# Optimization experiments

Measured on AMD Instinct MI355X. Metric: run time of the kernel, lower is better.

Reference implementation:

```python
import jax, jax.numpy as jnp
import numpy as np
import math

B, S, D = 4, 1024, 512
H, DK, DV = 8, 64, 64
NEG = -1.0e9
LN_EPS = 1e-5


def setup_inputs() -> dict:
    key = jax.random.key(0)
    ks = jax.random.split(key, 12)
    sc = 1.0 / math.sqrt(D)
    inp = {
        "input_Q": jax.random.normal(ks[0], (B, S, D), jnp.float32),
        "input_K": jax.random.normal(ks[1], (B, S, D), jnp.float32),
        "input_V": jax.random.normal(ks[2], (B, S, D), jnp.float32),
        "attn_mask": jax.random.randint(ks[3], (B, S, S), 0, 2).astype(bool),
        "bias_mask": jax.random.randint(ks[4], (B, S, S), 0, 2).astype(bool),
        "Wq": jax.random.normal(ks[5], (D, H * DK), jnp.float32) * sc,
        "Wk": jax.random.normal(ks[6], (D, H * DK), jnp.float32) * sc,
        "Wq2": jax.random.normal(ks[7], (D, H * DK), jnp.float32) * sc,
        "Wk2": jax.random.normal(ks[8], (D, H * DK), jnp.float32) * sc,
        "Wv": jax.random.normal(ks[9], (D, H * DV), jnp.float32) * sc,
        "Wo": jax.random.normal(ks[10], (H * DV, D), jnp.float32) * sc,
        "ln_g": jnp.ones((D,), jnp.float32),
        "ln_b": jnp.zeros((D,), jnp.float32),
    }
    return inp


def _heads(x, W, d):
    b, s, _ = x.shape
    return (x @ W).reshape(b, s, H, d).transpose(0, 2, 1, 3)  # [B,H,S,d]


def reference(input_Q, input_K, input_V, attn_mask, bias_mask,
              Wq, Wk, Wq2, Wk2, Wv, Wo, ln_g, ln_b):
    residual = input_Q
    Q = _heads(input_Q, Wq, DK)
    K = _heads(input_K, Wk, DK)
    V = _heads(input_V, Wv, DV)
    Q2 = _heads(input_Q, Wq2, DK)
    K2 = _heads(input_K, Wk2, DK)

    am = attn_mask[:, None, :, :]   # broadcast over heads
    bm = bias_mask[:, None, :, :]

    scores1 = jnp.einsum('bhqd,bhkd->bhqk', Q, K) / math.sqrt(DK)
    bias = jnp.einsum('bhqd,bhkd->bhqk', Q2, K2)
    bias = jnp.where(bm, NEG, bias)
    scores = jnp.where(am, NEG, scores1 + bias)
    attn = jax.nn.softmax(scores, axis=-1)          # [B,H,S,S]
    context = jnp.einsum('bhqk,bhkd->bhqd', attn, V)  # [B,H,S,DV]
    context = context.transpose(0, 2, 1, 3).reshape(B, S, H * DV)
    output = context @ Wo

    x = output + residual
    mu = jnp.mean(x, axis=-1, keepdims=True)
    var = jnp.mean(jnp.square(x - mu), axis=-1, keepdims=True)
    out = (x - mu) / jnp.sqrt(var + LN_EPS) * ln_g + ln_b
    return (out, attn)
```

## Files before the change

### kernel.cpp

```cpp
#include <hip/hip_runtime.h>
#include <hip/hip_fp16.h>

typedef _Float16 f16x8 __attribute__((ext_vector_type(8)));
typedef _Float16 f16x4 __attribute__((ext_vector_type(4)));
typedef float f32x4 __attribute__((ext_vector_type(4)));

__global__ __launch_bounds__(256) void wtrans6_kernel(
    const float* __restrict__ Wq, const float* __restrict__ Wk,
    const float* __restrict__ Wq2, const float* __restrict__ Wk2,
    const float* __restrict__ Wv, const float* __restrict__ Wo,
    __half* __restrict__ WqcT, __half* __restrict__ WkcT,
    __half* __restrict__ WvT, __half* __restrict__ WoT) {
  const float* src;
  __half* dst;
  float scale = 1.0f;
  switch (blockIdx.z) {
    case 0: src = Wq;  dst = WqcT;              scale = 0.125f; break;
    case 1: src = Wq2; dst = WqcT + 512 * 512;  break;
    case 2: src = Wk;  dst = WkcT;              break;
    case 3: src = Wk2; dst = WkcT + 512 * 512;  break;
    case 4: src = Wv;  dst = WvT;               break;
    default: src = Wo; dst = WoT;               break;
  }
  __shared__ float t[32][33];
  int n0 = blockIdx.x * 32, k0 = blockIdx.y * 32;
  int tx = threadIdx.x, ty = threadIdx.y;
#pragma unroll
  for (int i = 0; i < 4; i++)
    t[ty + i * 8][tx] = src[(size_t)(k0 + ty + i * 8) * 512 + n0 + tx];
  __syncthreads();
#pragma unroll
  for (int i = 0; i < 4; i++)
    dst[(size_t)(n0 + ty + i * 8) * 512 + k0 + tx] = __float2half(t[tx][ty + i * 8] * scale);
}

__global__ __launch_bounds__(128) void maskprep_kernel(const int* __restrict__ am,
                                                       const int* __restrict__ bm,
                                                       uint32_t* __restrict__ packed) {
  int bk = blockIdx.x;
  int w = bk & 3, bqt = bk >> 2, qt = bqt & 31, b = bqt >> 5;
  int t = threadIdx.x;
  int mi = t >> 6, lane = t & 63;
  int lg = lane >> 4, l15 = lane & 15;
  int qbase = qt * 32 + mi * 16 + lg * 4;
  int kbase = w * 256 + l15;
  uint32_t outw[4] = {0u, 0u, 0u, 0u};
#pragma unroll
  for (int kt = 0; kt < 16; kt++) {
    int k = kbase + kt * 16;
#pragma unroll
    for (int r = 0; r < 4; r++) {
      size_t idx = ((size_t)(b * 1024 + qbase + r)) * 1024 + k;
      uint32_t code = (am[idx] ? 1u : 0u) + (bm[idx] ? 1u : 0u);
      outw[kt >> 2] |= code << (((kt & 3) << 3) + (r << 1));
    }
  }
  uint4* dst = (uint4*)packed + ((size_t)bk * 64 + lane) * 2 + mi;
  *dst = make_uint4(outw[0], outw[1], outw[2], outw[3]);
}

template <int AF32>
__device__ __forceinline__ void gemm_body(const void* Ap, const __half* Bt, __half* C,
                                          int N, int bx, int by) {
  __shared__ __align__(16) _Float16 smem[10240];
  _Float16(*As)[40] = (_Float16(*)[40])smem;
  _Float16(*Bs)[40] = (_Float16(*)[40])(smem + 5120);
  int tid = threadIdx.x;
  int wave = tid >> 6, lane = tid & 63;
  int lg = lane >> 4, l15 = lane & 15;
  int wm = (wave >> 1) * 64, wn = (wave & 1) * 64;
  int bm0 = by * 128, bn0 = bx * 128;
  int srow = tid >> 1, sseg = (tid & 1) * 16;
  const float* Af = (const float*)Ap;
  const __half* Ah = (const __half*)Ap;
  f32x4 acc[4][4];
#pragma unroll
  for (int i = 0; i < 4; i++)
#pragma unroll
    for (int j = 0; j < 4; j++) acc[i][j] = (f32x4){0.f, 0.f, 0.f, 0.f};

  for (int kt = 0; kt < 16; kt++) {
    int k0 = kt * 32;
    if (AF32) {
      const float* s = Af + (size_t)(bm0 + srow) * 512 + k0 + sseg;
      _Float16* d = &As[srow][sseg];
#pragma unroll
      for (int i = 0; i < 16; i += 4) {
        float4 v = *(const float4*)(s + i);
        d[i] = (_Float16)v.x; d[i + 1] = (_Float16)v.y;
        d[i + 2] = (_Float16)v.z; d[i + 3] = (_Float16)v.w;
      }
    } else {
      const __half* s = Ah + (size_t)(bm0 + srow) * 512 + k0 + sseg;
      *(uint4*)&As[srow][sseg] = *(const uint4*)s;
      *(uint4*)(&As[srow][sseg] + 8) = *(const uint4*)(s + 8);
    }
    {
      const __half* s = Bt + (size_t)(bn0 + srow) * 512 + k0 + sseg;
      *(uint4*)&Bs[srow][sseg] = *(const uint4*)s;
      *(uint4*)(&Bs[srow][sseg] + 8) = *(const uint4*)(s + 8);
    }
    __syncthreads();
    f16x8 af[4], bf[4];
#pragma unroll
    for (int i = 0; i < 4; i++) af[i] = *(const f16x8*)&As[wm + i * 16 + l15][lg * 8];
#pragma unroll
    for (int j = 0; j < 4; j++) bf[j] = *(const f16x8*)&Bs[wn + j * 16 + l15][lg * 8];
#pragma unroll
    for (int i = 0; i < 4; i++)
#pragma unroll
      for (int j = 0; j < 4; j++)
        acc[i][j] = __builtin_amdgcn_mfma_f32_16x16x32_f16(af[i], bf[j], acc[i][j], 0, 0, 0);
    __syncthreads();
  }

  _Float16* cb = smem;
#pragma unroll
  for (int ph = 0; ph < 2; ph++) {
    __syncthreads();
    if ((wave >> 1) == ph) {
#pragma unroll
      for (int i = 0; i < 4; i++)
#pragma unroll
        for (int j = 0; j < 4; j++)
#pragma unroll
          for (int r = 0; r < 4; r++)
            cb[(i * 16 + lg * 4 + r) * 128 + wn + j * 16 + l15] =
                (_Float16)acc[i][j][r];
    }
    __syncthreads();
#pragma unroll
    for (int rr = 0; rr < 4; rr++) {
      int row = rr * 16 + (tid >> 4);
      int colh = (tid & 15) * 8;
      uint4 v = *(const uint4*)&cb[row * 128 + colh];
      *(uint4*)&C[(size_t)(bm0 + ph * 64 + row) * N + bn0 + colh] = v;
    }
  }
}

__global__ __launch_bounds__(256) void proj_kernel(
    const float* __restrict__ inQ, const float* __restrict__ inK,
    const float* __restrict__ inV, const __half* __restrict__ WqcT,
    const __half* __restrict__ WkcT, const __half* __restrict__ WvT,
    __half* __restrict__ QQ2, __half* __restrict__ KK2, __half* __restrict__ Vout) {
  int z = blockIdx.z;
  if (z == 0) {
    gemm_body<1>(inQ, WqcT, QQ2, 1024, blockIdx.x, blockIdx.y);
  } else if (z == 1) {
    gemm_body<1>(inK, WkcT, KK2, 1024, blockIdx.x, blockIdx.y);
  } else {
    if (blockIdx.x >= 4) return;
    gemm_body<1>(inV, WvT, Vout, 512, blockIdx.x, blockIdx.y);
  }
}

__global__ __launch_bounds__(256) void gemm_f16_kernel(const __half* __restrict__ A,
                                                       const __half* __restrict__ Bt,
                                                       __half* __restrict__ C, int N) {
  gemm_body<0>(A, Bt, C, N, blockIdx.x, blockIdx.y);
}

__global__ __launch_bounds__(256) void vtrans_kernel(const __half* __restrict__ V,
                                                     __half* __restrict__ Vt) {
  __shared__ __half t[64][72];
  int bh = blockIdx.y, b = bh >> 3, h = bh & 7;
  int s0 = blockIdx.x * 64;
  int tx = threadIdx.x, ty = threadIdx.y;
#pragma unroll
  for (int i = 0; i < 16; i++)
    t[ty + i * 4][tx] = V[(size_t)(b * 1024 + s0 + ty + i * 4) * 512 + h * 64 + tx];
  __syncthreads();
#pragma unroll
  for (int i = 0; i < 16; i++)
    Vt[((size_t)bh * 64 + ty + i * 4) * 1024 + s0 + tx] = t[tx][ty + i * 4];
}

__global__ __launch_bounds__(256, 2) void attn_kernel(
    const __half* __restrict__ QQ2, const __half* __restrict__ KK2,
    const __half* __restrict__ Vt, const uint32_t* __restrict__ packed,
    float* __restrict__ attn_out, __half* __restrict__ CTX) {
  int qt = blockIdx.x, bh = blockIdx.y;
  int b = bh >> 3, h = bh & 7;
  int q0 = qt * 32;
  int tid = threadIdx.x;
  int wave = tid >> 6, lane = tid & 63;
  int lg = lane >> 4, l15 = lane & 15;
  int kw = wave * 256;

  __shared__ __align__(16) _Float16 P[4][32][264];
  __shared__ float redmax[4][32], redsum[4][32];

  f16x8 qf[2][4];
  const __half* Qb = QQ2 + ((size_t)(b * 1024 + q0)) * 1024 + h * 64;
#pragma unroll
  for (int mi = 0; mi < 2; mi++)
#pragma unroll
    for (int ks = 0; ks < 4; ks++) {
      int off = (ks < 2) ? ks * 32 : 512 + (ks - 2) * 32;
      qf[mi][ks] = *(const f16x8*)(Qb + (size_t)(mi * 16 + l15) * 1024 + off + lg * 8);
    }

  uint4 mw[2];
  {
    const uint4* mp =
        (const uint4*)packed + ((size_t)((b * 32 + qt) * 4 + wave) * 64 + lane) * 2;
    mw[0] = mp[0];
    mw[1] = mp[1];
  }

  f16x4 sc16[2][16];
  float mx[2][4];
#pragma unroll
  for (int mi = 0; mi < 2; mi++)
#pragma unroll
    for (int r = 0; r < 4; r++) mx[mi][r] = -3.0e38f;
  const __half* Kb = KK2 + ((size_t)(b * 1024)) * 1024 + h * 64;
#pragma unroll
  for (int kt = 0; kt < 16; kt++) {
    int kc = kw + kt * 16;
    const __half* kp = Kb + (size_t)(kc + l15) * 1024 + lg * 8;
    f16x8 kf[4];
    kf[0] = *(const f16x8*)kp;
    kf[1] = *(const f16x8*)(kp + 32);
    kf[2] = *(const f16x8*)(kp + 512);
    kf[3] = *(const f16x8*)(kp + 544);
#pragma unroll
    for (int mi = 0; mi < 2; mi++) {
      f32x4 s = (f32x4){0.f, 0.f, 0.f, 0.f};
#pragma unroll
      for (int ks = 0; ks < 4; ks++)
        s = __builtin_amdgcn_mfma_f32_16x16x32_f16(qf[mi][ks], kf[ks], s, 0, 0, 0);
      uint32_t mword = ((const uint32_t*)&mw[mi])[kt >> 2];
      f16x4 sv;
#pragma unroll
      for (int r = 0; r < 4; r++) {
        uint32_t code = (mword >> (((kt & 3) << 3) + (r << 1))) & 3u;
        float sval = s[r] - 30000.0f * (float)code;
        sv[r] = (_Float16)sval;
        mx[mi][r] = fmaxf(mx[mi][r], (float)sv[r]);
      }
      sc16[mi][kt] = sv;
    }
  }

#pragma unroll
  for (int mi = 0; mi < 2; mi++)
#pragma unroll
    for (int r = 0; r < 4; r++) {
      float m = mx[mi][r];
#pragma unroll
      for (int o = 1; o < 16; o <<= 1) m = fmaxf(m, __shfl_xor(m, o));
      if (l15 == 0) redmax[wave][mi * 16 + lg * 4 + r] = m;
    }
  __syncthreads();
  float mfin[2][4];
#pragma unroll
  for (int mi = 0; mi < 2; mi++)
#pragma unroll
    for (int r = 0; r < 4; r++) {
      int row = mi * 16 + lg * 4 + r;
      mfin[mi][r] = fmaxf(fmaxf(redmax[0][row], redmax[1][row]),
                          fmaxf(redmax[2][row], redmax[3][row]));
    }

  float sm[2][4];
#pragma unroll
  for (int mi = 0; mi < 2; mi++)
#pragma unroll
    for (int r = 0; r < 4; r++) sm[mi][r] = 0.f;
#pragma unroll
  for (int kt = 0; kt < 16; kt++)
#pragma unroll
    for (int mi = 0; mi < 2; mi++) {
      f16x4 sv = sc16[mi][kt];
      f16x4 pv;
#pragma unroll
      for (int r = 0; r < 4; r++) {
        float p = __expf((float)sv[r] - mfin[mi][r]);
        sm[mi][r] += p;
        pv[r] = (_Float16)p;
      }
      sc16[mi][kt] = pv;
    }
#pragma unroll
  for (int mi = 0; mi < 2; mi++)
#pragma unroll
    for (int r = 0; r < 4; r++) {
      float s = sm[mi][r];
#pragma unroll
      for (int o = 1; o < 16; o <<= 1) s += __shfl_xor(s, o);
      if (l15 == 0) redsum[wave][mi * 16 + lg * 4 + r] = s;
    }
  __syncthreads();
  float inv[2][4];
#pragma unroll
  for (int mi = 0; mi < 2; mi++)
#pragma unroll
    for (int r = 0; r < 4; r++) {
      int row = mi * 16 + lg * 4 + r;
      inv[mi][r] =
          1.0f / (redsum[0][row] + redsum[1][row] + redsum[2][row] + redsum[3][row]);
    }

  float* ab = attn_out + ((size_t)bh * 1024 + q0) * 1024;
#pragma unroll
  for (int mi = 0; mi < 2; mi++)
#pragma unroll
    for (int kt = 0; kt < 16; kt++)
#pragma unroll
      for (int r = 0; r < 4; r++) {
        int row = mi * 16 + lg * 4 + r;
        int col = kw + kt * 16 + l15;
        float a = (float)sc16[mi][kt][r] * inv[mi][r];
        ab[(size_t)row * 1024 + col] = a;
        P[wave][row][kt * 16 + l15] = (_Float16)a;
      }
  __syncthreads();

  f32x4 ctx[2];
  ctx[0] = (f32x4){0.f, 0.f, 0.f, 0.f};
  ctx[1] = (f32x4){0.f, 0.f, 0.f, 0.f};
  const __half* Vb = Vt + (size_t)bh * 64 * 1024;
#pragma unroll
  for (int c = 0; c < 4; c++) {
    int kglob = c * 256;
#pragma unroll
    for (int kk = 0; kk < 8; kk++) {
      f16x8 pa0 = *(const f16x8*)&P[c][l15][kk * 32 + lg * 8];
      f16x8 pa1 = *(const f16x8*)&P[c][16 + l15][kk * 32 + lg * 8];
      f16x8 vf = *(const f16x8*)(Vb + (size_t)(wave * 16 + l15) * 1024 + kglob +
                                 kk * 32 + lg * 8);
      ctx[0] = __builtin_amdgcn_mfma_f32_16x16x32_f16(pa0, vf, ctx[0], 0, 0, 0);
      ctx[1] = __builtin_amdgcn_mfma_f32_16x16x32_f16(pa1, vf, ctx[1], 0, 0, 0);
    }
  }

#pragma unroll
  for (int mi = 0; mi < 2; mi++)
#pragma unroll
    for (int r = 0; r < 4; r++) {
      int row = mi * 16 + lg * 4 + r;
      CTX[(size_t)(b * 1024 + q0 + row) * 512 + h * 64 + wave * 16 + l15] =
          __float2half(ctx[mi][r]);
    }
}

__global__ __launch_bounds__(256) void ln_kernel(const __half* __restrict__ O,
                                                 const float* __restrict__ resid,
                                                 const float* __restrict__ g,
                                                 const float* __restrict__ bb,
                                                 float* __restrict__ out) {
  int row = blockIdx.x, tid = threadIdx.x;
  int wv = tid >> 6, lane = tid & 63;
  size_t base = (size_t)row * 512;
  float x0 = __half2float(O[base + tid]) + resid[base + tid];
  float x1 = __half2float(O[base + tid + 256]) + resid[base + tid + 256];
  __shared__ float red[4];
  float s = x0 + x1;
#pragma unroll
  for (int o = 1; o < 64; o <<= 1) s += __shfl_xor(s, o);
  if (lane == 0) red[wv] = s;
  __syncthreads();
  float mean = (red[0] + red[1] + red[2] + red[3]) * (1.0f / 512.0f);
  __syncthreads();
  float d0 = x0 - mean, d1 = x1 - mean;
  float v = d0 * d0 + d1 * d1;
#pragma unroll
  for (int o = 1; o < 64; o <<= 1) v += __shfl_xor(v, o);
  if (lane == 0) red[wv] = v;
  __syncthreads();
  float var = (red[0] + red[1] + red[2] + red[3]) * (1.0f / 512.0f);
  float rs = rsqrtf(var + 1e-5f);
  __builtin_nontemporal_store(d0 * rs * g[tid] + bb[tid], out + base + tid);
  __builtin_nontemporal_store(d1 * rs * g[tid + 256] + bb[tid + 256],
                              out + base + tid + 256);
}

extern "C" void kernel_launch(void* const* d_in, const int* in_sizes, int n_in,
                              void* d_out, int out_size, void* d_ws, size_t ws_size,
                              hipStream_t stream) {
  const float* inQ = (const float*)d_in[0];
  const float* inK = (const float*)d_in[1];
  const float* inV = (const float*)d_in[2];
  const int* am = (const int*)d_in[3];
  const int* bmk = (const int*)d_in[4];
  const float* Wq = (const float*)d_in[5];
  const float* Wk = (const float*)d_in[6];
  const float* Wq2 = (const float*)d_in[7];
  const float* Wk2 = (const float*)d_in[8];
  const float* Wv = (const float*)d_in[9];
  const float* Wo = (const float*)d_in[10];
  const float* lng = (const float*)d_in[11];
  const float* lnb = (const float*)d_in[12];

  char* ws = (char*)d_ws;
  __half* WqcT = (__half*)ws; ws += (size_t)1024 * 512 * 2;
  __half* WkcT = (__half*)ws; ws += (size_t)1024 * 512 * 2;
  __half* WvT = (__half*)ws;  ws += (size_t)512 * 512 * 2;
  __half* WoT = (__half*)ws;  ws += (size_t)512 * 512 * 2;
  __half* QQ2 = (__half*)ws;  ws += (size_t)4096 * 1024 * 2;
  __half* KK2 = (__half*)ws;  ws += (size_t)4096 * 1024 * 2;
  __half* Vout = (__half*)ws; ws += (size_t)4096 * 512 * 2;
  __half* Vt = (__half*)ws;   ws += (size_t)4096 * 512 * 2;
  __half* CTX = (__half*)ws;  ws += (size_t)4096 * 512 * 2;
  __half* Obuf = (__half*)ws; ws += (size_t)4096 * 512 * 2;
  uint32_t* packed = (uint32_t*)Obuf;

  float* out0 = (float*)d_out;
  float* attn_out = out0 + (size_t)4 * 1024 * 512;

  wtrans6_kernel<<<dim3(16, 16, 6), dim3(32, 8), 0, stream>>>(Wq, Wk, Wq2, Wk2, Wv, Wo,
                                                              WqcT, WkcT, WvT, WoT);
  maskprep_kernel<<<512, 128, 0, stream>>>(am, bmk, packed);
  proj_kernel<<<dim3(8, 32, 3), 256, 0, stream>>>(inQ, inK, inV, WqcT, WkcT, WvT, QQ2,
                                                  KK2, Vout);
  vtrans_kernel<<<dim3(16, 32), dim3(64, 4), 0, stream>>>(Vout, Vt);
  attn_kernel<<<dim3(32, 32), 256, 0, stream>>>(QQ2, KK2, Vt, packed, attn_out, CTX);
  gemm_f16_kernel<<<dim3(4, 32), 256, 0, stream>>>(CTX, WoT, Obuf, 512);
  ln_kernel<<<4096, 256, 0, stream>>>(Obuf, inQ, lng, lnb, out0);
}
```

Measured before the change: 152.8 us.

## Fuse V transpose and mask packing into projection kernel; one-wave-per-row layernorm

```diff
diff --git a/kernel.cpp b/kernel.cpp
--- a/kernel.cpp
+++ b/kernel.cpp
@@ -34,12 +34,11 @@
     dst[(size_t)(n0 + ty + i * 8) * 512 + k0 + tx] = __float2half(t[tx][ty + i * 8] * scale);
 }
 
-__global__ __launch_bounds__(128) void maskprep_kernel(const int* __restrict__ am,
-                                                       const int* __restrict__ bm,
-                                                       uint32_t* __restrict__ packed) {
-  int bk = blockIdx.x;
+__device__ __forceinline__ void maskprep_body(const int* __restrict__ am,
+                                              const int* __restrict__ bm,
+                                              uint32_t* __restrict__ packed, int bk,
+                                              int t) {
   int w = bk & 3, bqt = bk >> 2, qt = bqt & 31, b = bqt >> 5;
-  int t = threadIdx.x;
   int mi = t >> 6, lane = t & 63;
   int lg = lane >> 4, l15 = lane & 15;
   int qbase = qt * 32 + mi * 16 + lg * 4;
@@ -61,7 +60,8 @@
 
 template <int AF32>
 __device__ __forceinline__ void gemm_body(const void* Ap, const __half* Bt, __half* C,
-                                          int N, int bx, int by) {
+                                          int N, int bx, int by, int vt,
+                                          __half* __restrict__ vtp) {
   __shared__ __align__(16) _Float16 smem[10240];
   _Float16(*As)[40] = (_Float16(*)[40])smem;
   _Float16(*Bs)[40] = (_Float16(*)[40])(smem + 5120);
@@ -129,12 +129,29 @@
                 (_Float16)acc[i][j][r];
     }
     __syncthreads();
-#pragma unroll
-    for (int rr = 0; rr < 4; rr++) {
-      int row = rr * 16 + (tid >> 4);
-      int colh = (tid & 15) * 8;
-      uint4 v = *(const uint4*)&cb[row * 128 + colh];
-      *(uint4*)&C[(size_t)(bm0 + ph * 64 + row) * N + bn0 + colh] = v;
+    if (!vt) {
+#pragma unroll
+      for (int rr = 0; rr < 4; rr++) {
+        int row = rr * 16 + (tid >> 4);
+        int colh = (tid & 15) * 8;
+        uint4 v = *(const uint4*)&cb[row * 128 + colh];
+        *(uint4*)&C[(size_t)(bm0 + ph * 64 + row) * N + bn0 + colh] = v;
+      }
+    } else {
+      int m0 = bm0 + ph * 64;
+      int b = m0 >> 10, s0 = m0 & 1023;
+      int dvc = tid >> 1;
+      int sh = tid & 1;
+      int bh = b * 8 + bx * 2 + (dvc >> 6);
+      int dv = dvc & 63;
+      __half* dst = vtp + ((size_t)bh * 64 + dv) * 1024 + s0 + sh * 32;
+#pragma unroll
+      for (int g = 0; g < 4; g++) {
+        f16x8 v;
+#pragma unroll
+        for (int k = 0; k < 8; k++) v[k] = cb[(sh * 32 + g * 8 + k) * 128 + dvc];
+        *(f16x8*)(dst + g * 8) = v;
+      }
     }
   }
 }
@@ -143,37 +160,27 @@
     const float* __restrict__ inQ, const float* __restrict__ inK,
     const float* __restrict__ inV, const __half* __restrict__ WqcT,
     const __half* __restrict__ WkcT, const __half* __restrict__ WvT,
-    __half* __restrict__ QQ2, __half* __restrict__ KK2, __half* __restrict__ Vout) {
+    const int* __restrict__ am, const int* __restrict__ bm,
+    __half* __restrict__ QQ2, __half* __restrict__ KK2, __half* __restrict__ Vt,
+    uint32_t* __restrict__ packed) {
   int z = blockIdx.z;
   if (z == 0) {
-    gemm_body<1>(inQ, WqcT, QQ2, 1024, blockIdx.x, blockIdx.y);
+    gemm_body<1>(inQ, WqcT, QQ2, 1024, blockIdx.x, blockIdx.y, 0, nullptr);
   } else if (z == 1) {
-    gemm_body<1>(inK, WkcT, KK2, 1024, blockIdx.x, blockIdx.y);
+    gemm_body<1>(inK, WkcT, KK2, 1024, blockIdx.x, blockIdx.y, 0, nullptr);
+  } else if (z == 2) {
+    if (blockIdx.x >= 4) return;
+    gemm_body<1>(inV, WvT, nullptr, 512, blockIdx.x, blockIdx.y, 1, Vt);
   } else {
-    if (blockIdx.x >= 4) return;
-    gemm_body<1>(inV, WvT, Vout, 512, blockIdx.x, blockIdx.y);
+    int bk = (blockIdx.y * 8 + blockIdx.x) * 2 + (threadIdx.x >> 7);
+    maskprep_body(am, bm, packed, bk, threadIdx.x & 127);
   }
 }
 
 __global__ __launch_bounds__(256) void gemm_f16_kernel(const __half* __restrict__ A,
                                                        const __half* __restrict__ Bt,
                                                        __half* __restrict__ C, int N) {
-  gemm_body<0>(A, Bt, C, N, blockIdx.x, blockIdx.y);
-}
-
-__global__ __launch_bounds__(256) void vtrans_kernel(const __half* __restrict__ V,
-                                                     __half* __restrict__ Vt) {
-  __shared__ __half t[64][72];
-  int bh = blockIdx.y, b = bh >> 3, h = bh & 7;
-  int s0 = blockIdx.x * 64;
-  int tx = threadIdx.x, ty = threadIdx.y;
-#pragma unroll
-  for (int i = 0; i < 16; i++)
-    t[ty + i * 4][tx] = V[(size_t)(b * 1024 + s0 + ty + i * 4) * 512 + h * 64 + tx];
-  __syncthreads();
-#pragma unroll
-  for (int i = 0; i < 16; i++)
-    Vt[((size_t)bh * 64 + ty + i * 4) * 1024 + s0 + tx] = t[tx][ty + i * 4];
+  gemm_body<0>(A, Bt, C, N, blockIdx.x, blockIdx.y, 0, nullptr);
 }
 
 __global__ __launch_bounds__(256, 2) void attn_kernel(
@@ -351,30 +358,39 @@
                                                  const float* __restrict__ g,
                                                  const float* __restrict__ bb,
                                                  float* __restrict__ out) {
-  int row = blockIdx.x, tid = threadIdx.x;
-  int wv = tid >> 6, lane = tid & 63;
-  size_t base = (size_t)row * 512;
-  float x0 = __half2float(O[base + tid]) + resid[base + tid];
-  float x1 = __half2float(O[base + tid + 256]) + resid[base + tid + 256];
-  __shared__ float red[4];
-  float s = x0 + x1;
+  int w = threadIdx.x >> 6, lane = threadIdx.x & 63;
+  int row = blockIdx.x * 4 + w;
+  size_t base = (size_t)row * 512 + lane * 8;
+  f16x8 ov = *(const f16x8*)(O + base);
+  float4 r0 = *(const float4*)(resid + base);
+  float4 r1 = *(const float4*)(resid + base + 4);
+  float x[8];
+  x[0] = (float)ov[0] + r0.x; x[1] = (float)ov[1] + r0.y;
+  x[2] = (float)ov[2] + r0.z; x[3] = (float)ov[3] + r0.w;
+  x[4] = (float)ov[4] + r1.x; x[5] = (float)ov[5] + r1.y;
+  x[6] = (float)ov[6] + r1.z; x[7] = (float)ov[7] + r1.w;
+  float s = 0.f;
+#pragma unroll
+  for (int i = 0; i < 8; i++) s += x[i];
 #pragma unroll
   for (int o = 1; o < 64; o <<= 1) s += __shfl_xor(s, o);
-  if (lane == 0) red[wv] = s;
-  __syncthreads();
-  float mean = (red[0] + red[1] + red[2] + red[3]) * (1.0f / 512.0f);
-  __syncthreads();
-  float d0 = x0 - mean, d1 = x1 - mean;
-  float v = d0 * d0 + d1 * d1;
+  float mean = s * (1.0f / 512.0f);
+  float d[8], v = 0.f;
+#pragma unroll
+  for (int i = 0; i < 8; i++) { d[i] = x[i] - mean; v += d[i] * d[i]; }
 #pragma unroll
   for (int o = 1; o < 64; o <<= 1) v += __shfl_xor(v, o);
-  if (lane == 0) red[wv] = v;
-  __syncthreads();
-  float var = (red[0] + red[1] + red[2] + red[3]) * (1.0f / 512.0f);
-  float rs = rsqrtf(var + 1e-5f);
-  __builtin_nontemporal_store(d0 * rs * g[tid] + bb[tid], out + base + tid);
-  __builtin_nontemporal_store(d1 * rs * g[tid + 256] + bb[tid + 256],
-                              out + base + tid + 256);
+  float rs = rsqrtf(v * (1.0f / 512.0f) + 1e-5f);
+  float4 g0 = *(const float4*)(g + lane * 8);
+  float4 g1 = *(const float4*)(g + lane * 8 + 4);
+  float4 b0 = *(const float4*)(bb + lane * 8);
+  float4 b1 = *(const float4*)(bb + lane * 8 + 4);
+  f32x4 o0 = {d[0] * rs * g0.x + b0.x, d[1] * rs * g0.y + b0.y,
+              d[2] * rs * g0.z + b0.z, d[3] * rs * g0.w + b0.w};
+  f32x4 o1 = {d[4] * rs * g1.x + b1.x, d[5] * rs * g1.y + b1.y,
+              d[6] * rs * g1.z + b1.z, d[7] * rs * g1.w + b1.w};
+  __builtin_nontemporal_store(o0, (f32x4*)(out + base));
+  __builtin_nontemporal_store(o1, (f32x4*)(out + base + 4));
 }
 
 extern "C" void kernel_launch(void* const* d_in, const int* in_sizes, int n_in,
@@ -401,7 +417,6 @@
   __half* WoT = (__half*)ws;  ws += (size_t)512 * 512 * 2;
   __half* QQ2 = (__half*)ws;  ws += (size_t)4096 * 1024 * 2;
   __half* KK2 = (__half*)ws;  ws += (size_t)4096 * 1024 * 2;
-  __half* Vout = (__half*)ws; ws += (size_t)4096 * 512 * 2;
   __half* Vt = (__half*)ws;   ws += (size_t)4096 * 512 * 2;
   __half* CTX = (__half*)ws;  ws += (size_t)4096 * 512 * 2;
   __half* Obuf = (__half*)ws; ws += (size_t)4096 * 512 * 2;
@@ -412,11 +427,9 @@
 
   wtrans6_kernel<<<dim3(16, 16, 6), dim3(32, 8), 0, stream>>>(Wq, Wk, Wq2, Wk2, Wv, Wo,
                                                               WqcT, WkcT, WvT, WoT);
-  maskprep_kernel<<<512, 128, 0, stream>>>(am, bmk, packed);
-  proj_kernel<<<dim3(8, 32, 3), 256, 0, stream>>>(inQ, inK, inV, WqcT, WkcT, WvT, QQ2,
-                                                  KK2, Vout);
-  vtrans_kernel<<<dim3(16, 32), dim3(64, 4), 0, stream>>>(Vout, Vt);
+  proj_kernel<<<dim3(8, 32, 4), 256, 0, stream>>>(inQ, inK, inV, WqcT, WkcT, WvT, am,
+                                                  bmk, QQ2, KK2, Vt, packed);
   attn_kernel<<<dim3(32, 32), 256, 0, stream>>>(QQ2, KK2, Vt, packed, attn_out, CTX);
   gemm_f16_kernel<<<dim3(4, 32), 256, 0, stream>>>(CTX, WoT, Obuf, 512);
-  ln_kernel<<<4096, 256, 0, stream>>>(Obuf, inQ, lng, lnb, out0);
-}
+  ln_kernel<<<1024, 256, 0, stream>>>(Obuf, inQ, lng, lnb, out0);
+}
```

New measurement: 138.3 us. 1.11x faster.
